# Optimization experiments

Hardware: AMD Instinct MI355X
Metric: run time of the kernel (lower is better)

The kernel has to match this reference:

```python
import jax, jax.numpy as jnp
import numpy as np

TEMPERATURE = 8.0  # sqrt(head_dim=64)
NEG_INF = -1e9


def setup_inputs() -> dict:
    key = jax.random.key(0)
    kq, kk, kv, km = jax.random.split(key, 4)
    B, H, S, D = 2, 16, 2048, 64
    q = jax.random.normal(kq, (B, H, S, D), dtype=jnp.float32)
    k = jax.random.normal(kk, (B, H, S, D), dtype=jnp.float32)
    v = jax.random.normal(kv, (B, H, S, D), dtype=jnp.float32)
    mask = jax.random.randint(km, (B, 1, 1, S), 0, 2, dtype=jnp.int32)
    return {"q": q, "k": k, "v": v, "mask": mask}


def reference(q, k, v, mask):
    # attn = (q / T) @ k^T  -> [B,H,S,S]
    scores = jnp.einsum("bhqd,bhkd->bhqk", q / TEMPERATURE, k)
    scores = jnp.where(mask == 0, NEG_INF, scores)
    attn = jax.nn.softmax(scores, axis=-1)  # dropout is identity in eval mode
    output = jnp.einsum("bhqk,bhkd->bhqd", attn, v)
    return (output, attn)
```

## Files before the change

### kernel.cpp

```cpp
#include <hip/hip_runtime.h>
#include <stdint.h>

constexpr int S   = 2048;
constexpr int D   = 64;
constexpr int BH  = 32;
constexpr int QT  = 64;
constexpr int KT  = 64;
constexpr int LDP = 72;

using short8  = __attribute__((ext_vector_type(8))) short;
using float4v = __attribute__((ext_vector_type(4))) float;

static __device__ __forceinline__ unsigned short f2bf(float f) {
    union { float f; unsigned u; } x; x.f = f;
    unsigned u = x.u;
    u += 0x7fffu + ((u >> 16) & 1u);
    return (unsigned short)(u >> 16);
}

__global__ __launch_bounds__(256) void vt_kernel(const float* __restrict__ v,
                                                 unsigned short* __restrict__ vt) {
    __shared__ __align__(16) unsigned short sT[64][LDP];
    const int blk = blockIdx.x;
    const int bh  = blk >> 5;
    const int k0  = (blk & 31) << 6;
    const int t   = threadIdx.x;
    const float* vp = v + ((size_t)bh * S + k0) * D;
#pragma unroll
    for (int i = 0; i < 4; ++i) {
        const int f4 = t + 256 * i;
        float4v val = ((const float4v*)vp)[f4];
        const int e = f4 * 4;
        const int r = e >> 6;
        const int c = e & 63;
        sT[c + 0][r] = f2bf(val.x);
        sT[c + 1][r] = f2bf(val.y);
        sT[c + 2][r] = f2bf(val.z);
        sT[c + 3][r] = f2bf(val.w);
    }
    __syncthreads();
#pragma unroll
    for (int i = 0; i < 2; ++i) {
        const int f    = t + 256 * i;
        const int drow = f >> 3;
        const int kc   = (f & 7) * 8;
        short8 val = *(const short8*)&sT[drow][kc];
        *(short8*)(vt + ((size_t)bh * D + drow) * S + k0 + kc) = val;
    }
}

__global__ __launch_bounds__(256, 4) void attn_kernel(const float* __restrict__ q,
                                                      const float* __restrict__ k,
                                                      const int* __restrict__ mask,
                                                      const unsigned short* __restrict__ vt,
                                                      float* __restrict__ out) {
    __shared__ __align__(16) unsigned short sQ[QT][LDP];
    __shared__ __align__(16) unsigned short sK[KT][LDP];
    __shared__ __align__(16) unsigned short sVt[D][LDP];
    __shared__ __align__(16) unsigned short sP[4][16][LDP];

    const int tid  = threadIdx.x;
    const int wave = tid >> 6;
    const int lane = tid & 63;
    const int quad = lane >> 4;
    const int n16  = lane & 15;

    const int bx = blockIdx.x;
    const int bh = bx >> 5;
    const int qt = bx & 31;
    const int q0 = qt * QT;
    const int b  = bh >> 4;

    const float* qp = q + (size_t)bh * S * D;
    const float* kp = k + (size_t)bh * S * D;
    const unsigned short* vtp = vt + (size_t)bh * D * S;
    const int* mp = mask + b * S;

    {
        const float4v* src = (const float4v*)(qp + (size_t)q0 * D);
#pragma unroll
        for (int i = 0; i < 4; ++i) {
            const int f4 = tid + 256 * i;
            float4v val = src[f4];
            const int e = f4 * 4;
            const int row = e >> 6, col = e & 63;
            ushort4 pk;
            pk.x = f2bf(val.x * 0.125f);
            pk.y = f2bf(val.y * 0.125f);
            pk.z = f2bf(val.z * 0.125f);
            pk.w = f2bf(val.w * 0.125f);
            *(ushort4*)&sQ[row][col] = pk;
        }
    }
    __syncthreads();

    const short8 aq0 = *(const short8*)&sQ[wave * 16 + n16][quad * 8];
    const short8 aq1 = *(const short8*)&sQ[wave * 16 + n16][32 + quad * 8];

    float4v accO[4];
    const float4v zero4 = {0.f, 0.f, 0.f, 0.f};
#pragma unroll
    for (int nv = 0; nv < 4; ++nv) accO[nv] = zero4;
    float lsum[4] = {0.f, 0.f, 0.f, 0.f};

    for (int kt = 0; kt < S / KT; ++kt) {
        const int k0 = kt * KT;
        __syncthreads();
        {
            const float4v* src = (const float4v*)(kp + (size_t)k0 * D);
#pragma unroll
            for (int i = 0; i < 4; ++i) {
                const int f4 = tid + 256 * i;
                float4v val = src[f4];
                const int e = f4 * 4;
                const int row = e >> 6, col = e & 63;
                ushort4 pk;
                pk.x = f2bf(val.x);
                pk.y = f2bf(val.y);
                pk.z = f2bf(val.z);
                pk.w = f2bf(val.w);
                *(ushort4*)&sK[row][col] = pk;
            }
#pragma unroll
            for (int i = 0; i < 2; ++i) {
                const int f    = tid + 256 * i;
                const int drow = f >> 3;
                const int kc8  = (f & 7) * 8;
                short8 val = *(const short8*)(vtp + (size_t)drow * S + k0 + kc8);
                *(short8*)&sVt[drow][kc8] = val;
            }
        }
        __syncthreads();

        float4v cf[4];
#pragma unroll
        for (int nc = 0; nc < 4; ++nc) cf[nc] = zero4;
#pragma unroll
        for (int c = 0; c < 2; ++c) {
            const short8 a = (c == 0) ? aq0 : aq1;
#pragma unroll
            for (int nc = 0; nc < 4; ++nc) {
                const short8 bfr = *(const short8*)&sK[nc * 16 + n16][c * 32 + quad * 8];
                cf[nc] = __builtin_amdgcn_mfma_f32_16x16x32_bf16(a, bfr, cf[nc], 0, 0, 0);
            }
        }

        float pv_[4][4];
#pragma unroll
        for (int nc = 0; nc < 4; ++nc) {
            const float mv = (float)mp[k0 + nc * 16 + n16];
#pragma unroll
            for (int r = 0; r < 4; ++r)
                pv_[nc][r] = __expf(cf[nc][r]) * mv;
        }
#pragma unroll
        for (int r = 0; r < 4; ++r) {
            float s = pv_[0][r] + pv_[1][r] + pv_[2][r] + pv_[3][r];
            s += __shfl_xor(s, 1, 64);
            s += __shfl_xor(s, 2, 64);
            s += __shfl_xor(s, 4, 64);
            s += __shfl_xor(s, 8, 64);
            lsum[r] += s;
        }
#pragma unroll
        for (int nc = 0; nc < 4; ++nc)
#pragma unroll
            for (int r = 0; r < 4; ++r)
                sP[wave][quad * 4 + r][nc * 16 + n16] = f2bf(pv_[nc][r]);
        __syncthreads();

#pragma unroll
        for (int kc = 0; kc < 2; ++kc) {
            const short8 ap = *(const short8*)&sP[wave][n16][kc * 32 + quad * 8];
#pragma unroll
            for (int nv = 0; nv < 4; ++nv) {
                const short8 bv = *(const short8*)&sVt[nv * 16 + n16][kc * 32 + quad * 8];
                accO[nv] = __builtin_amdgcn_mfma_f32_16x16x32_bf16(ap, bv, accO[nv], 0, 0, 0);
            }
        }
    }

    float linv[4];
#pragma unroll
    for (int r = 0; r < 4; ++r) linv[r] = 1.0f / lsum[r];

    {
        const size_t obase = ((size_t)bh * S + q0 + wave * 16) * D;
#pragma unroll
        for (int nv = 0; nv < 4; ++nv)
#pragma unroll
            for (int r = 0; r < 4; ++r)
                out[obase + (size_t)(quad * 4 + r) * D + nv * 16 + n16] = accO[nv][r] * linv[r];
    }

    float* attn = out + (size_t)BH * S * D;
    const size_t abase = (size_t)bh * S * S + (size_t)(q0 + wave * 16) * S;
    for (int kt = 0; kt < S / KT; ++kt) {
        const int k0 = kt * KT;
        __syncthreads();
        {
            const float4v* src = (const float4v*)(kp + (size_t)k0 * D);
#pragma unroll
            for (int i = 0; i < 4; ++i) {
                const int f4 = tid + 256 * i;
                float4v val = src[f4];
                const int e = f4 * 4;
                const int row = e >> 6, col = e & 63;
                ushort4 pk;
                pk.x = f2bf(val.x);
                pk.y = f2bf(val.y);
                pk.z = f2bf(val.z);
                pk.w = f2bf(val.w);
                *(ushort4*)&sK[row][col] = pk;
            }
        }
        __syncthreads();

        float4v cf[4];
#pragma unroll
        for (int nc = 0; nc < 4; ++nc) cf[nc] = zero4;
#pragma unroll
        for (int c = 0; c < 2; ++c) {
            const short8 a = (c == 0) ? aq0 : aq1;
#pragma unroll
            for (int nc = 0; nc < 4; ++nc) {
                const short8 bfr = *(const short8*)&sK[nc * 16 + n16][c * 32 + quad * 8];
                cf[nc] = __builtin_amdgcn_mfma_f32_16x16x32_bf16(a, bfr, cf[nc], 0, 0, 0);
            }
        }
#pragma unroll
        for (int nc = 0; nc < 4; ++nc) {
            const float mv = (float)mp[k0 + nc * 16 + n16];
#pragma unroll
            for (int r = 0; r < 4; ++r) {
                const float val = __expf(cf[nc][r]) * mv * linv[r];
                attn[abase + (size_t)(quad * 4 + r) * S + k0 + nc * 16 + n16] = val;
            }
        }
    }
}

extern "C" void kernel_launch(void* const* d_in, const int* in_sizes, int n_in,
                              void* d_out, int out_size, void* d_ws, size_t ws_size,
                              hipStream_t stream) {
    const float* q    = (const float*)d_in[0];
    const float* k    = (const float*)d_in[1];
    const float* v    = (const float*)d_in[2];
    const int*   mask = (const int*)d_in[3];
    unsigned short* vt = (unsigned short*)d_ws;
    float* out = (float*)d_out;

    vt_kernel<<<dim3(BH * (S / 64)), dim3(256), 0, stream>>>(v, vt);
    attn_kernel<<<dim3(BH * (S / QT)), dim3(256), 0, stream>>>(q, k, mask, vt, out);
}
```

Measured before the change: 719.7 us.

## Precompute bf16 K and swizzled V tiles, read K from global, double-buffer V via LDS-DMA

A prep kernel now converts K to bf16 with an XOR-swizzled layout and writes V transposed as contiguous swizzled 64x64 tiles. The attention kernel loads Q fragments straight into registers, reads K MFMA operands directly from global/L2 instead of staging them through LDS, and double-buffers V tiles with global_load_lds asynchronous copies. This removes the per-tile fp32-to-bf16 conversion of K in both passes and most of the block-wide barriers. The trade-off is more global/L2 traffic for K reads and reliance on waitcnt ordering instead of explicit barriers, which may be fragile around the LDS-DMA completion.

```diff
diff --git a/kernel.cpp b/kernel.cpp
--- a/kernel.cpp
+++ b/kernel.cpp
@@ -1,101 +1,114 @@
 #include <hip/hip_runtime.h>
 #include <stdint.h>
+
+typedef unsigned short ushort_t;
 
 constexpr int S   = 2048;
 constexpr int D   = 64;
 constexpr int BH  = 32;
 constexpr int QT  = 64;
 constexpr int KT  = 64;
-constexpr int LDP = 72;
+constexpr int NT  = S / KT;
 
 using short8  = __attribute__((ext_vector_type(8))) short;
 using float4v = __attribute__((ext_vector_type(4))) float;
 
-static __device__ __forceinline__ unsigned short f2bf(float f) {
+static __device__ __forceinline__ ushort_t f2bf(float f) {
     union { float f; unsigned u; } x; x.f = f;
     unsigned u = x.u;
     u += 0x7fffu + ((u >> 16) & 1u);
-    return (unsigned short)(u >> 16);
-}
-
-__global__ __launch_bounds__(256) void vt_kernel(const float* __restrict__ v,
-                                                 unsigned short* __restrict__ vt) {
-    __shared__ __align__(16) unsigned short sT[64][LDP];
+    return (ushort_t)(u >> 16);
+}
+
+static __device__ __forceinline__ void gload_lds16(const void* g, void* l) {
+    __builtin_amdgcn_global_load_lds(
+        (const __attribute__((address_space(1))) void*)g,
+        (__attribute__((address_space(3))) void*)l, 16, 0, 0);
+}
+
+__global__ __launch_bounds__(256) void prep_kernel(const float* __restrict__ k,
+                                                   const float* __restrict__ v,
+                                                   ushort_t* __restrict__ kb,
+                                                   ushort_t* __restrict__ vtb) {
+    __shared__ __align__(16) ushort_t sT[64][72];
     const int blk = blockIdx.x;
     const int bh  = blk >> 5;
-    const int k0  = (blk & 31) << 6;
+    const int kt  = blk & 31;
+    const int t0  = kt << 6;
     const int t   = threadIdx.x;
-    const float* vp = v + ((size_t)bh * S + k0) * D;
+    const size_t base = ((size_t)bh * S + t0) * D;
+    const float4v* ksrc = (const float4v*)(k + base);
+    const float4v* vsrc = (const float4v*)(v + base);
 #pragma unroll
     for (int i = 0; i < 4; ++i) {
         const int f4 = t + 256 * i;
-        float4v val = ((const float4v*)vp)[f4];
-        const int e = f4 * 4;
-        const int r = e >> 6;
-        const int c = e & 63;
-        sT[c + 0][r] = f2bf(val.x);
-        sT[c + 1][r] = f2bf(val.y);
-        sT[c + 2][r] = f2bf(val.z);
-        sT[c + 3][r] = f2bf(val.w);
+        const int e  = f4 * 4;
+        const int row = e >> 6, col = e & 63;
+        float4v kv = ksrc[f4];
+        ushort4 pk;
+        pk.x = f2bf(kv.x); pk.y = f2bf(kv.y); pk.z = f2bf(kv.z); pk.w = f2bf(kv.w);
+        const int sw = (((col >> 3) ^ (row & 7)) << 3) | (col & 7);
+        *(ushort4*)(kb + base + (size_t)row * 64 + sw) = pk;
+        float4v vv = vsrc[f4];
+        sT[col + 0][row] = f2bf(vv.x);
+        sT[col + 1][row] = f2bf(vv.y);
+        sT[col + 2][row] = f2bf(vv.z);
+        sT[col + 3][row] = f2bf(vv.w);
     }
     __syncthreads();
 #pragma unroll
     for (int i = 0; i < 2; ++i) {
-        const int f    = t + 256 * i;
-        const int drow = f >> 3;
-        const int kc   = (f & 7) * 8;
-        short8 val = *(const short8*)&sT[drow][kc];
-        *(short8*)(vt + ((size_t)bh * D + drow) * S + k0 + kc) = val;
+        const int f  = t + 256 * i;
+        const int d  = f >> 3;
+        const int ch = f & 7;
+        short8 val = *(const short8*)&sT[d][ch * 8];
+        *(short8*)(vtb + ((size_t)bh * 32 + kt) * 4096 + d * 64 + ((ch ^ (d & 7)) << 3)) = val;
     }
 }
 
 __global__ __launch_bounds__(256, 4) void attn_kernel(const float* __restrict__ q,
-                                                      const float* __restrict__ k,
+                                                      const ushort_t* __restrict__ kb,
+                                                      const ushort_t* __restrict__ vtb,
                                                       const int* __restrict__ mask,
-                                                      const unsigned short* __restrict__ vt,
                                                       float* __restrict__ out) {
-    __shared__ __align__(16) unsigned short sQ[QT][LDP];
-    __shared__ __align__(16) unsigned short sK[KT][LDP];
-    __shared__ __align__(16) unsigned short sVt[D][LDP];
-    __shared__ __align__(16) unsigned short sP[4][16][LDP];
+    __shared__ __align__(16) ushort_t sVt[2][4096];
+    __shared__ __align__(16) ushort_t sP[4][16][72];
 
     const int tid  = threadIdx.x;
     const int wave = tid >> 6;
     const int lane = tid & 63;
     const int quad = lane >> 4;
     const int n16  = lane & 15;
+    const int h8   = n16 & 7;
 
     const int bx = blockIdx.x;
     const int bh = bx >> 5;
-    const int qt = bx & 31;
-    const int q0 = qt * QT;
+    const int q0 = (bx & 31) * QT;
     const int b  = bh >> 4;
 
-    const float* qp = q + (size_t)bh * S * D;
-    const float* kp = k + (size_t)bh * S * D;
-    const unsigned short* vtp = vt + (size_t)bh * D * S;
+    const ushort_t* kbp = kb + (size_t)bh * S * D;
+    const ushort_t* vtp = vtb + (size_t)bh * 32 * 4096;
     const int* mp = mask + b * S;
 
+    short8 aq0, aq1;
     {
-        const float4v* src = (const float4v*)(qp + (size_t)q0 * D);
-#pragma unroll
-        for (int i = 0; i < 4; ++i) {
-            const int f4 = tid + 256 * i;
-            float4v val = src[f4];
-            const int e = f4 * 4;
-            const int row = e >> 6, col = e & 63;
-            ushort4 pk;
-            pk.x = f2bf(val.x * 0.125f);
-            pk.y = f2bf(val.y * 0.125f);
-            pk.z = f2bf(val.z * 0.125f);
-            pk.w = f2bf(val.w * 0.125f);
-            *(ushort4*)&sQ[row][col] = pk;
-        }
-    }
-    __syncthreads();
-
-    const short8 aq0 = *(const short8*)&sQ[wave * 16 + n16][quad * 8];
-    const short8 aq1 = *(const short8*)&sQ[wave * 16 + n16][32 + quad * 8];
+        const float* qrow = q + (size_t)bh * S * D + (size_t)(q0 + wave * 16 + n16) * D;
+        float4v a = *(const float4v*)(qrow + quad * 8);
+        float4v bb = *(const float4v*)(qrow + quad * 8 + 4);
+        float4v c = *(const float4v*)(qrow + 32 + quad * 8);
+        float4v d = *(const float4v*)(qrow + 32 + quad * 8 + 4);
+        aq0[0] = (short)f2bf(a.x * 0.125f); aq0[1] = (short)f2bf(a.y * 0.125f);
+        aq0[2] = (short)f2bf(a.z * 0.125f); aq0[3] = (short)f2bf(a.w * 0.125f);
+        aq0[4] = (short)f2bf(bb.x * 0.125f); aq0[5] = (short)f2bf(bb.y * 0.125f);
+        aq0[6] = (short)f2bf(bb.z * 0.125f); aq0[7] = (short)f2bf(bb.w * 0.125f);
+        aq1[0] = (short)f2bf(c.x * 0.125f); aq1[1] = (short)f2bf(c.y * 0.125f);
+        aq1[2] = (short)f2bf(c.z * 0.125f); aq1[3] = (short)f2bf(c.w * 0.125f);
+        aq1[4] = (short)f2bf(d.x * 0.125f); aq1[5] = (short)f2bf(d.y * 0.125f);
+        aq1[6] = (short)f2bf(d.z * 0.125f); aq1[7] = (short)f2bf(d.w * 0.125f);
+    }
+
+    const int swz0 = ((0 * 4 + quad) ^ h8) << 3;
+    const int swz1 = ((1 * 4 + quad) ^ h8) << 3;
 
     float4v accO[4];
     const float4v zero4 = {0.f, 0.f, 0.f, 0.f};
@@ -103,46 +116,39 @@
     for (int nv = 0; nv < 4; ++nv) accO[nv] = zero4;
     float lsum[4] = {0.f, 0.f, 0.f, 0.f};
 
-    for (int kt = 0; kt < S / KT; ++kt) {
+    {
+        const ushort_t* vtile = vtp;
+#pragma unroll
+        for (int i = 0; i < 2; ++i) {
+            const int off = (wave * 2 + i) * 512;
+            gload_lds16(vtile + off + lane * 8, &sVt[0][off]);
+        }
+    }
+
+    for (int kt = 0; kt < NT; ++kt) {
         const int k0 = kt * KT;
+        const int buf = kt & 1;
         __syncthreads();
-        {
-            const float4v* src = (const float4v*)(kp + (size_t)k0 * D);
-#pragma unroll
-            for (int i = 0; i < 4; ++i) {
-                const int f4 = tid + 256 * i;
-                float4v val = src[f4];
-                const int e = f4 * 4;
-                const int row = e >> 6, col = e & 63;
-                ushort4 pk;
-                pk.x = f2bf(val.x);
-                pk.y = f2bf(val.y);
-                pk.z = f2bf(val.z);
-                pk.w = f2bf(val.w);
-                *(ushort4*)&sK[row][col] = pk;
+        if (kt + 1 < NT) {
+            const ushort_t* vtile = vtp + (size_t)(kt + 1) * 4096;
+#pragma unroll
+            for (int i = 0; i < 2; ++i) {
+                const int off = (wave * 2 + i) * 512;
+                gload_lds16(vtile + off + lane * 8, &sVt[buf ^ 1][off]);
             }
-#pragma unroll
-            for (int i = 0; i < 2; ++i) {
-                const int f    = tid + 256 * i;
-                const int drow = f >> 3;
-                const int kc8  = (f & 7) * 8;
-                short8 val = *(const short8*)(vtp + (size_t)drow * S + k0 + kc8);
-                *(short8*)&sVt[drow][kc8] = val;
-            }
-        }
-        __syncthreads();
+        }
 
         float4v cf[4];
 #pragma unroll
         for (int nc = 0; nc < 4; ++nc) cf[nc] = zero4;
-#pragma unroll
-        for (int c = 0; c < 2; ++c) {
-            const short8 a = (c == 0) ? aq0 : aq1;
-#pragma unroll
-            for (int nc = 0; nc < 4; ++nc) {
-                const short8 bfr = *(const short8*)&sK[nc * 16 + n16][c * 32 + quad * 8];
-                cf[nc] = __builtin_amdgcn_mfma_f32_16x16x32_bf16(a, bfr, cf[nc], 0, 0, 0);
-            }
+        const ushort_t* ktile = kbp + (size_t)k0 * 64;
+#pragma unroll
+        for (int nc = 0; nc < 4; ++nc) {
+            const ushort_t* krow = ktile + (size_t)(nc * 16 + n16) * 64;
+            short8 b0 = *(const short8*)(krow + swz0);
+            short8 b1 = *(const short8*)(krow + swz1);
+            cf[nc] = __builtin_amdgcn_mfma_f32_16x16x32_bf16(aq0, b0, cf[nc], 0, 0, 0);
+            cf[nc] = __builtin_amdgcn_mfma_f32_16x16x32_bf16(aq1, b1, cf[nc], 0, 0, 0);
         }
 
         float pv_[4][4];
@@ -167,14 +173,15 @@
 #pragma unroll
             for (int r = 0; r < 4; ++r)
                 sP[wave][quad * 4 + r][nc * 16 + n16] = f2bf(pv_[nc][r]);
-        __syncthreads();
+        asm volatile("s_waitcnt lgkmcnt(0)" ::: "memory");
 
 #pragma unroll
         for (int kc = 0; kc < 2; ++kc) {
             const short8 ap = *(const short8*)&sP[wave][n16][kc * 32 + quad * 8];
+            const int sw = (kc == 0) ? swz0 : swz1;
 #pragma unroll
             for (int nv = 0; nv < 4; ++nv) {
-                const short8 bv = *(const short8*)&sVt[nv * 16 + n16][kc * 32 + quad * 8];
+                const short8 bv = *(const short8*)&sVt[buf][(nv * 16 + n16) * 64 + sw];
                 accO[nv] = __builtin_amdgcn_mfma_f32_16x16x32_bf16(ap, bv, accO[nv], 0, 0, 0);
             }
         }
@@ -183,7 +190,6 @@
     float linv[4];
 #pragma unroll
     for (int r = 0; r < 4; ++r) linv[r] = 1.0f / lsum[r];
-
     {
         const size_t obase = ((size_t)bh * S + q0 + wave * 16) * D;
 #pragma unroll
@@ -195,38 +201,19 @@
 
     float* attn = out + (size_t)BH * S * D;
     const size_t abase = (size_t)bh * S * S + (size_t)(q0 + wave * 16) * S;
-    for (int kt = 0; kt < S / KT; ++kt) {
+    for (int kt = 0; kt < NT; ++kt) {
         const int k0 = kt * KT;
-        __syncthreads();
-        {
-            const float4v* src = (const float4v*)(kp + (size_t)k0 * D);
-#pragma unroll
-            for (int i = 0; i < 4; ++i) {
-                const int f4 = tid + 256 * i;
-                float4v val = src[f4];
-                const int e = f4 * 4;
-                const int row = e >> 6, col = e & 63;
-                ushort4 pk;
-                pk.x = f2bf(val.x);
-                pk.y = f2bf(val.y);
-                pk.z = f2bf(val.z);
-                pk.w = f2bf(val.w);
-                *(ushort4*)&sK[row][col] = pk;
-            }
-        }
-        __syncthreads();
-
         float4v cf[4];
 #pragma unroll
         for (int nc = 0; nc < 4; ++nc) cf[nc] = zero4;
-#pragma unroll
-        for (int c = 0; c < 2; ++c) {
-            const short8 a = (c == 0) ? aq0 : aq1;
-#pragma unroll
-            for (int nc = 0; nc < 4; ++nc) {
-                const short8 bfr = *(const short8*)&sK[nc * 16 + n16][c * 32 + quad * 8];
-                cf[nc] = __builtin_amdgcn_mfma_f32_16x16x32_bf16(a, bfr, cf[nc], 0, 0, 0);
-            }
+        const ushort_t* ktile = kbp + (size_t)k0 * 64;
+#pragma unroll
+        for (int nc = 0; nc < 4; ++nc) {
+            const ushort_t* krow = ktile + (size_t)(nc * 16 + n16) * 64;
+            short8 b0 = *(const short8*)(krow + swz0);
+            short8 b1 = *(const short8*)(krow + swz1);
+            cf[nc] = __builtin_amdgcn_mfma_f32_16x16x32_bf16(aq0, b0, cf[nc], 0, 0, 0);
+            cf[nc] = __builtin_amdgcn_mfma_f32_16x16x32_bf16(aq1, b1, cf[nc], 0, 0, 0);
         }
 #pragma unroll
         for (int nc = 0; nc < 4; ++nc) {
@@ -247,9 +234,10 @@
     const float* k    = (const float*)d_in[1];
     const float* v    = (const float*)d_in[2];
     const int*   mask = (const int*)d_in[3];
-    unsigned short* vt = (unsigned short*)d_ws;
+    ushort_t* kb  = (ushort_t*)d_ws;
+    ushort_t* vtb = (ushort_t*)((char*)d_ws + (size_t)BH * S * D * 2);
     float* out = (float*)d_out;
 
-    vt_kernel<<<dim3(BH * (S / 64)), dim3(256), 0, stream>>>(v, vt);
-    attn_kernel<<<dim3(BH * (S / QT)), dim3(256), 0, stream>>>(q, k, mask, vt, out);
-}
+    prep_kernel<<<dim3(BH * NT), dim3(256), 0, stream>>>(k, v, kb, vtb);
+    attn_kernel<<<dim3(BH * (S / QT)), dim3(256), 0, stream>>>(q, kb, vtb, mask, out);
+}
```

Result: slower. 743.9 us (+3.4%).
